# Kernel tuning notes

Measured on AMD Instinct MI355X. Metric: run time of the kernel, lower is better.

The kernel has to match this reference:

```python
import jax, jax.numpy as jnp
import numpy as np

DIM, N_HEADS, N_KV, HEAD_DIM = 3072, 24, 8, 128
N_REP = N_HEADS // N_KV  # 3
ROPE_THETA = 500000.0
B, S = 2, 2048


def _rope_tables(seqlen, head_dim, theta):
    inv = 1.0 / (theta ** (np.arange(0, head_dim, 2, dtype=np.float32) / head_dim))
    t = np.arange(seqlen, dtype=np.float32)
    ang = np.outer(t, inv)  # [S, head_dim//2]
    return jnp.asarray(np.cos(ang)), jnp.asarray(np.sin(ang))


def setup_inputs() -> dict:
    key = jax.random.key(0)
    ks = jax.random.split(key, 5)
    sd = 1.0 / np.sqrt(DIM)
    x = jax.random.normal(ks[0], (B, S, DIM), jnp.float32)
    wq = jax.random.normal(ks[1], (DIM, N_HEADS * HEAD_DIM), jnp.float32) * sd
    wk = jax.random.normal(ks[2], (DIM, N_KV * HEAD_DIM), jnp.float32) * sd
    wv = jax.random.normal(ks[3], (DIM, N_KV * HEAD_DIM), jnp.float32) * sd
    wo = jax.random.normal(ks[4], (N_HEADS * HEAD_DIM, DIM), jnp.float32) * sd
    fc, fs = _rope_tables(S, HEAD_DIM, ROPE_THETA)
    return {"x": x, "wq": wq, "wk": wk, "wv": wv, "wo": wo,
            "freqs_cos": fc, "freqs_sin": fs}


def _apply_rope(t, cos, sin):
    # t: [B,S,H,hd]; cos/sin: [S, hd//2]. Complex mult on (even, odd) pairs.
    tr = t[..., 0::2]
    ti = t[..., 1::2]
    cos = cos[None, :, None, :]
    sin = sin[None, :, None, :]
    out_r = tr * cos - ti * sin
    out_i = tr * sin + ti * cos
    return jnp.stack([out_r, out_i], axis=-1).reshape(t.shape)


def reference(x, wq, wk, wv, wo, freqs_cos, freqs_sin):
    b, s, _ = x.shape
    xq = (x @ wq).reshape(b, s, N_HEADS, HEAD_DIM)
    xk = (x @ wk).reshape(b, s, N_KV, HEAD_DIM)
    xv = (x @ wv).reshape(b, s, N_KV, HEAD_DIM)
    xq = _apply_rope(xq, freqs_cos, freqs_sin)
    xk = _apply_rope(xk, freqs_cos, freqs_sin)

    # GQA without materializing repeated k/v: q head h maps to kv group h // N_REP
    q = xq.reshape(b, s, N_KV, N_REP, HEAD_DIM)
    scale = 1.0 / np.sqrt(HEAD_DIM)
    scores = jnp.einsum('bsgrd,btgd->bgrst', q, xk) * scale  # [B,KV,rep,S,S]
    causal = jnp.tril(jnp.ones((s, s), dtype=bool))
    scores = jnp.where(causal[None, None, None], scores, jnp.finfo(scores.dtype).min)
    probs = jax.nn.softmax(scores, axis=-1)
    out = jnp.einsum('bgrst,btgd->bsgrd', probs, xv).reshape(b, s, N_HEADS * HEAD_DIM)
    return out @ wo
```

## Files before the change

### kernel.cpp

```cpp
#include <hip/hip_runtime.h>
#include <hip/hip_bf16.h>

typedef __hip_bfloat16 bf16;
typedef __bf16 bf16x8 __attribute__((ext_vector_type(8)));
typedef float f32x4 __attribute__((ext_vector_type(4)));
typedef short short8 __attribute__((ext_vector_type(8)));

#define NH 24
#define NKV 8
#define HD 128
#define SEQ 2048
#define NREP 3
#define QKVD 5120
#define KOFF 3072
#define VOFF 4096

__device__ inline void gload16(const void* g, void* l) {
  __builtin_amdgcn_global_load_lds(
      (const __attribute__((address_space(1))) void*)g,
      (__attribute__((address_space(3))) void*)l, 16, 0, 0);
}

__global__ void cast_f32_bf16(const float* __restrict__ in, bf16* __restrict__ out, int n4) {
  int i = blockIdx.x * 256 + threadIdx.x;
  if (i >= n4) return;
  float4 v = reinterpret_cast<const float4*>(in)[i];
  ushort4 u;
  u.x = __builtin_bit_cast(unsigned short, __float2bfloat16(v.x));
  u.y = __builtin_bit_cast(unsigned short, __float2bfloat16(v.y));
  u.z = __builtin_bit_cast(unsigned short, __float2bfloat16(v.z));
  u.w = __builtin_bit_cast(unsigned short, __float2bfloat16(v.w));
  reinterpret_cast<ushort4*>(out)[i] = u;
}

__global__ void transpose_cast(const float* __restrict__ W, bf16* __restrict__ WT, int K, int N) {
  __shared__ bf16 tile[32][33];
  int n0 = blockIdx.x * 32, k0 = blockIdx.y * 32;
  int tx = threadIdx.x, ty = threadIdx.y;
#pragma unroll
  for (int i = 0; i < 4; ++i) {
    int kl = ty + i * 8;
    tile[kl][tx] = __float2bfloat16(W[(size_t)(k0 + kl) * N + n0 + tx]);
  }
  __syncthreads();
#pragma unroll
  for (int i = 0; i < 4; ++i) {
    int nl = ty + i * 8;
    WT[(size_t)(n0 + nl) * K + k0 + tx] = tile[tx][nl];
  }
}

__global__ void transpose_v(const bf16* __restrict__ Vsrc, bf16* __restrict__ Vt) {
  __shared__ bf16 tile[32][33];
  int bg = blockIdx.z;
  int b = bg >> 3, g = bg & 7;
  int s0 = blockIdx.x * 32, d0 = blockIdx.y * 32;
  int tx = threadIdx.x, ty = threadIdx.y;
#pragma unroll
  for (int i = 0; i < 4; ++i) {
    int sl = ty + i * 8;
    tile[sl][tx] = Vsrc[(size_t)(b * SEQ + s0 + sl) * QKVD + g * HD + d0 + tx];
  }
  __syncthreads();
#pragma unroll
  for (int i = 0; i < 4; ++i) {
    int dl = ty + i * 8;
    Vt[((size_t)(b * NKV + g) * HD + d0 + dl) * SEQ + s0 + tx] = tile[tx][dl];
  }
}

__global__ void rope_kernel(bf16* __restrict__ T, const float* __restrict__ cosT,
                            const float* __restrict__ sinT, int H, int stride, int total) {
  int i = blockIdx.x * 256 + threadIdx.x;
  if (i >= total) return;
  int d2 = i & 63;
  int rh = i >> 6;
  int r = rh / H;
  int h = rh - r * H;
  int s = r & (SEQ - 1);
  float c = cosT[s * 64 + d2];
  float sn = sinT[s * 64 + d2];
  bf16* p = T + (size_t)r * stride + h * HD + d2 * 2;
  float a = __bfloat162float(p[0]);
  float b = __bfloat162float(p[1]);
  p[0] = __float2bfloat16(a * c - b * sn);
  p[1] = __float2bfloat16(a * sn + b * c);
}

#define QSLOT 14336
__global__ __launch_bounds__(512, 1) void gemm_qkv(const bf16* __restrict__ A,
                                                   const bf16* __restrict__ BT,
                                                   bf16* __restrict__ C,
                                                   int M, int N, int K, int gx) {
  extern __shared__ __align__(16) bf16 ls[];
  int nwg = gridDim.x;
  int flat = blockIdx.x;
  int swz = (flat & 7) * (nwg >> 3) + (flat >> 3);
  int bx = swz % gx, by = swz / gx;
  int m0 = by * 128, n0 = bx * 320;
  int tid = threadIdx.x, w = tid >> 6, lane = tid & 63;
  int wm = w >> 2, wn = w & 3;
  int lr = lane & 15, lk = lane >> 4;

  int aoff, adst;
  {
    int t = tid;
    int row = t >> 2, c = t & 3;
    aoff = row * K + ((c ^ ((row >> 1) & 3)) * 8);
    adst = t * 8;
  }
  const int nb = (tid < 256) ? 3 : 2;
  const int bbase = (tid < 256) ? tid : 768 + (tid - 256);
  int boff[3], bdst[3];
#pragma unroll
  for (int i = 0; i < 3; ++i) {
    int t = bbase + i * 256;
    if (t >= 1280) t = 0;
    int row = t >> 2, c = t & 3;
    boff[i] = row * K + ((c ^ ((row >> 1) & 3)) * 8);
    bdst[i] = 4096 + t * 8;
  }
  const bf16* Ab = A + (size_t)m0 * K;
  const bf16* Bb = BT + (size_t)n0 * K;

  auto STAGE_A = [&](int kt, int h, int slot) {
    const bf16* s = Ab + kt * 64 + h * 32;
    gload16(s + aoff, ls + slot * QSLOT + adst);
  };
  auto STAGE_B = [&](int kt, int h, int slot) {
    const bf16* s = Bb + kt * 64 + h * 32;
    bf16* d = ls + slot * QSLOT;
#pragma unroll
    for (int i = 0; i < 3; ++i)
      if (i < nb) gload16(s + boff[i], d + bdst[i]);
  };
  auto WAITN = [&] {
    if (tid < 256) asm volatile("s_waitcnt vmcnt(4)" ::: "memory");
    else           asm volatile("s_waitcnt vmcnt(3)" ::: "memory");
  };

  f32x4 acc[4][5] = {};
  bf16x8 aF[2], bF[5];

  auto LDA = [&](int slot, int mh) {
    const bf16* base = ls + slot * QSLOT;
#pragma unroll
    for (int mt = 0; mt < 2; ++mt) {
      int row = wm * 64 + (mh * 2 + mt) * 16 + lr;
      aF[mt] = *reinterpret_cast<const bf16x8*>(&base[row * 32 + ((lk ^ ((row >> 1) & 3)) * 8)]);
    }
  };
  auto LDB = [&](int slot) {
    const bf16* base = ls + slot * QSLOT + 4096;
#pragma unroll
    for (int nt = 0; nt < 5; ++nt) {
      int row = wn * 80 + nt * 16 + lr;
      bF[nt] = *reinterpret_cast<const bf16x8*>(&base[row * 32 + ((lk ^ ((row >> 1) & 3)) * 8)]);
    }
  };

#define PHASE(CSLOT, MH, STAGE_EXPR, DO_WAIT)                                       \
  {                                                                                 \
    __builtin_amdgcn_sched_barrier(0);                                              \
    if (MH == 0) LDB(CSLOT);                                                        \
    LDA(CSLOT, MH);                                                                 \
    STAGE_EXPR;                                                                     \
    __builtin_amdgcn_s_barrier();                                                   \
    asm volatile("s_waitcnt lgkmcnt(0)" ::: "memory");                              \
    __builtin_amdgcn_sched_barrier(0);                                              \
    __builtin_amdgcn_s_setprio(1);                                                  \
    _Pragma("unroll") for (int mt = 0; mt < 2; ++mt)                                \
        _Pragma("unroll") for (int nt = 0; nt < 5; ++nt)                            \
            acc[MH * 2 + mt][nt] =                                                  \
        __builtin_amdgcn_mfma_f32_16x16x32_bf16(aF[mt], bF[nt], acc[MH * 2 + mt][nt], 0, 0, 0); \
    __builtin_amdgcn_s_setprio(0);                                                  \
    if (DO_WAIT) WAITN();                                                           \
    __builtin_amdgcn_sched_barrier(0);                                              \
    __builtin_amdgcn_s_barrier();                                                   \
  }

  const int KT = K >> 6;
  const int IT = KT >> 1;

  STAGE_A(0, 0, 0); STAGE_B(0, 0, 0);
  STAGE_A(0, 1, 1); STAGE_B(0, 1, 1);
  STAGE_A(1, 0, 2); STAGE_B(1, 0, 2);
  WAITN();
  __builtin_amdgcn_s_barrier();

  for (int j = 0; j < IT; ++j) {
    int k1 = 2 * j + 1;
    int k2 = 2 * j + 2 < KT ? 2 * j + 2 : KT - 1;
    int k3 = 2 * j + 3 < KT ? 2 * j + 3 : KT - 1;
    PHASE(0, 0, STAGE_A(k1, 1, 3), false)
    PHASE(0, 1, STAGE_B(k1, 1, 3), false)
    PHASE(1, 0, STAGE_A(k2, 0, 0), false)
    PHASE(1, 1, STAGE_B(k2, 0, 0), true)
    PHASE(2, 0, STAGE_A(k2, 1, 1), false)
    PHASE(2, 1, STAGE_B(k2, 1, 1), false)
    PHASE(3, 0, STAGE_A(k3, 0, 2), false)
    PHASE(3, 1, STAGE_B(k3, 0, 2), true)
  }
  asm volatile("s_waitcnt vmcnt(0)" ::: "memory");
#undef PHASE

#pragma unroll
  for (int fr = 0; fr < 4; ++fr)
#pragma unroll
    for (int nt = 0; nt < 5; ++nt)
#pragma unroll
      for (int r = 0; r < 4; ++r) {
        int m = m0 + wm * 64 + fr * 16 + lk * 4 + r;
        int n = n0 + wn * 80 + nt * 16 + lr;
        C[(size_t)m * N + n] = __float2bfloat16(acc[fr][nt][r]);
      }
}

template <int NF, bool OUT_BF16>
__global__ __launch_bounds__(512, 1) void gemm_bt4(const bf16* __restrict__ A,
                                                   const bf16* __restrict__ BT,
                                                   void* __restrict__ Cv,
                                                   int M, int N, int K, int gx) {
  constexpr int BN = 64 * NF;
  constexpr int ASZ = 256 * 32;
  constexpr int BSZ = BN * 32;
  constexpr int SLOT = ASZ + BSZ;
  constexpr int HI = (NF + 1) / 2;
  extern __shared__ __align__(16) bf16 ls[];
  int nwg = gridDim.x;
  int flat = blockIdx.x;
  int swz = (flat & 7) * (nwg >> 3) + (flat >> 3);
  int bx = swz % gx, by = swz / gx;
  int m0 = by * 256, n0 = bx * BN;
  int tid = threadIdx.x, w = tid >> 6, lane = tid & 63;
  int wm = w >> 2, wn = w & 3;
  int lr = lane & 15, lk = lane >> 4;

  int aoff[2], adst[2];
#pragma unroll
  for (int i = 0; i < 2; ++i) {
    int t = i * 512 + tid;
    int row = t >> 2, c = t & 3;
    aoff[i] = row * K + ((c ^ ((row >> 1) & 3)) * 8);
    adst[i] = t * 8;
  }
  const int nb = (tid < 256) ? HI : NF / 2;
  const int bbase = (tid < 256) ? tid : HI * 256 + (tid - 256);
  int boff[HI], bdst[HI];
#pragma unroll
  for (int i = 0; i < HI; ++i) {
    int t = bbase + i * 256;
    if (t >= 256 * NF) t = 0;
    int row = t >> 2, c = t & 3;
    boff[i] = row * K + ((c ^ ((row >> 1) & 3)) * 8);
    bdst[i] = ASZ + t * 8;
  }
  const bf16* Ab = A + (size_t)m0 * K;
  const bf16* Bb = BT + (size_t)n0 * K;

  auto STAGE_A = [&](int kt, int h, int slot) {
    const bf16* s = Ab + kt * 64 + h * 32;
    bf16* d = ls + slot * SLOT;
#pragma unroll
    for (int i = 0; i < 2; ++i) gload16(s + aoff[i], d + adst[i]);
  };
  auto STAGE_B = [&](int kt, int h, int slot) {
    const bf16* s = Bb + kt * 64 + h * 32;
    bf16* d = ls + slot * SLOT;
#pragma unroll
    for (int i = 0; i < HI; ++i)
      if (i < nb) gload16(s + boff[i], d + bdst[i]);
  };
  auto WAITN = [&] {
    if (tid < 256) asm volatile("s_waitcnt vmcnt(4)" ::: "memory");
    else           asm volatile("s_waitcnt vmcnt(3)" ::: "memory");
  };

  f32x4 acc[8][NF] = {};
  bf16x8 aF[4], bF[NF];

  auto LDA = [&](int slot, int mh) {
    const bf16* base = ls + slot * SLOT;
#pragma unroll
    for (int mt = 0; mt < 4; ++mt) {
      int row = wm * 128 + (mh * 4 + mt) * 16 + lr;
      aF[mt] = *reinterpret_cast<const bf16x8*>(&base[row * 32 + ((lk ^ ((row >> 1) & 3)) * 8)]);
    }
  };
  auto LDB = [&](int slot) {
    const bf16* base = ls + slot * SLOT + ASZ;
#pragma unroll
    for (int nt = 0; nt < NF; ++nt) {
      int row = wn * (16 * NF) + nt * 16 + lr;
      bF[nt] = *reinterpret_cast<const bf16x8*>(&base[row * 32 + ((lk ^ ((row >> 1) & 3)) * 8)]);
    }
  };

#define PHASE(CSLOT, MH, STAGE_EXPR, DO_WAIT)                                       \
  {                                                                                 \
    __builtin_amdgcn_sched_barrier(0);                                              \
    if (MH == 0) LDB(CSLOT);                                                        \
    LDA(CSLOT, MH);                                                                 \
    STAGE_EXPR;                                                                     \
    __builtin_amdgcn_s_barrier();                                                   \
    asm volatile("s_waitcnt lgkmcnt(0)" ::: "memory");                              \
    __builtin_amdgcn_sched_barrier(0);                                              \
    __builtin_amdgcn_s_setprio(1);                                                  \
    _Pragma("unroll") for (int mt = 0; mt < 4; ++mt)                                \
        _Pragma("unroll") for (int nt = 0; nt < NF; ++nt)                           \
            acc[MH * 4 + mt][nt] =                                                  \
        __builtin_amdgcn_mfma_f32_16x16x32_bf16(aF[mt], bF[nt], acc[MH * 4 + mt][nt], 0, 0, 0); \
    __builtin_amdgcn_s_setprio(0);                                                  \
    if (DO_WAIT) WAITN();                                                           \
    __builtin_amdgcn_sched_barrier(0);                                              \
    __builtin_amdgcn_s_barrier();                                                   \
  }

  const int KT = K >> 6;
  const int IT = KT >> 1;

  STAGE_A(0, 0, 0); STAGE_B(0, 0, 0);
  STAGE_A(0, 1, 1); STAGE_B(0, 1, 1);
  STAGE_A(1, 0, 2); STAGE_B(1, 0, 2);
  WAITN();
  __builtin_amdgcn_s_barrier();

  for (int j = 0; j < IT; ++j) {
    int k1 = 2 * j + 1;
    int k2 = 2 * j + 2 < KT ? 2 * j + 2 : KT - 1;
    int k3 = 2 * j + 3 < KT ? 2 * j + 3 : KT - 1;
    PHASE(0, 0, STAGE_A(k1, 1, 3), false)
    PHASE(0, 1, STAGE_B(k1, 1, 3), false)
    PHASE(1, 0, STAGE_A(k2, 0, 0), false)
    PHASE(1, 1, STAGE_B(k2, 0, 0), true)
    PHASE(2, 0, STAGE_A(k2, 1, 1), false)
    PHASE(2, 1, STAGE_B(k2, 1, 1), false)
    PHASE(3, 0, STAGE_A(k3, 0, 2), false)
    PHASE(3, 1, STAGE_B(k3, 0, 2), true)
  }
  asm volatile("s_waitcnt vmcnt(0)" ::: "memory");
#undef PHASE

#pragma unroll
  for (int fr = 0; fr < 8; ++fr)
#pragma unroll
    for (int nt = 0; nt < NF; ++nt)
#pragma unroll
      for (int r = 0; r < 4; ++r) {
        int m = m0 + wm * 128 + fr * 16 + lk * 4 + r;
        int n = n0 + wn * (16 * NF) + nt * 16 + lr;
        float v = acc[fr][nt][r];
        if (OUT_BF16)
          reinterpret_cast<bf16*>(Cv)[(size_t)m * N + n] = __float2bfloat16(v);
        else
          reinterpret_cast<float*>(Cv)[(size_t)m * N + n] = v;
      }
}

#define SCALE_LOG2 0.12751745f

__global__ __launch_bounds__(256, 3) void attn_kernel(const bf16* __restrict__ QKV,
                                                      const bf16* __restrict__ Vt,
                                                      bf16* __restrict__ O) {
  __shared__ bf16 Klds[64 * 128];
  __shared__ bf16 Vlds[128 * 64];
  __shared__ bf16 Plds[4][16 * 64];
  int bh = blockIdx.y;
  int b = bh / NH, h = bh % NH, g = h / NREP;
  int tid = threadIdx.x, w = tid >> 6, lane = tid & 63;
  int lr = lane & 15, lk = lane >> 4;
  const int NT = SEQ / 64;

  const bf16* kvK = QKV + ((size_t)b * SEQ) * QKVD + KOFF + g * HD;
  const bf16* kvVt = Vt + ((size_t)(b * NKV + g) * HD) * SEQ;
  int koff[4];
  bf16* kdst[4];
#pragma unroll
  for (int i = 0; i < 4; ++i) {
    int t = i * 256 + tid;
    int row = t >> 4, c = t & 15;
    int sc = c ^ (row & 7);
    koff[i] = row * QKVD + sc * 8;
    kdst[i] = Klds + t * 8;
  }
  int voff[4];
  bf16* vdst[4];
#pragma unroll
  for (int i = 0; i < 4; ++i) {
    int t = i * 256 + tid;
    int d = t >> 3, c = t & 7;
    int sc = c ^ (d & 7);
    voff[i] = d * SEQ + sc * 8;
    vdst[i] = Vlds + t * 8;
  }

  bf16* pb = Plds[w];

#pragma unroll 1
  for (int pass = 0; pass < 2; ++pass) {
    int qt = pass ? (NT - 1 - (int)blockIdx.x) : (int)blockIdx.x;
    int q0 = qt * 64 + w * 16;

    bf16x8 aQ[4];
    {
      const bf16* qrow = QKV + ((size_t)(b * SEQ) + q0 + lr) * QKVD + h * HD;
#pragma unroll
      for (int kk = 0; kk < 4; ++kk)
        aQ[kk] = *reinterpret_cast<const bf16x8*>(qrow + kk * 32 + lk * 8);
    }

    f32x4 Oacc[8] = {};
    float m_s[4], l_s[4];
#pragma unroll
    for (int r = 0; r < 4; ++r) { m_s[r] = -1e30f; l_s[r] = 0.f; }

    int jlast = qt * 64;
    for (int j0 = 0; j0 <= jlast; j0 += 64) {
      __syncthreads();
      {
        const bf16* ks = kvK + (size_t)j0 * QKVD;
        const bf16* vs = kvVt + j0;
#pragma unroll
        for (int i = 0; i < 4; ++i) gload16(ks + koff[i], kdst[i]);
#pragma unroll
        for (int i = 0; i < 4; ++i) gload16(vs + voff[i], vdst[i]);
      }
      __syncthreads();
      if (j0 > q0 + 15) continue;

      f32x4 sc4[4] = {};
#pragma unroll
      for (int kk = 0; kk < 4; ++kk) {
#pragma unroll
        for (int nt = 0; nt < 4; ++nt) {
          int jrow = nt * 16 + lr;
          int pos = (4 * kk + lk) ^ (lr & 7);
          bf16x8 bK = *reinterpret_cast<const bf16x8*>(&Klds[jrow * 128 + pos * 8]);
          sc4[nt] = __builtin_amdgcn_mfma_f32_16x16x32_bf16(aQ[kk], bK, sc4[nt], 0, 0, 0);
        }
      }

      float sv[4][4], mx[4];
#pragma unroll
      for (int r = 0; r < 4; ++r) mx[r] = -3e38f;
#pragma unroll
      for (int nt = 0; nt < 4; ++nt) {
        int col = j0 + nt * 16 + lr;
#pragma unroll
        for (int r = 0; r < 4; ++r) {
          int row = q0 + lk * 4 + r;
          sv[nt][r] = (col > row) ? -3e38f : sc4[nt][r] * SCALE_LOG2;
          mx[r] = fmaxf(mx[r], sv[nt][r]);
        }
      }
#pragma unroll
      for (int d = 1; d < 16; d <<= 1)
#pragma unroll
        for (int r = 0; r < 4; ++r) mx[r] = fmaxf(mx[r], __shfl_xor(mx[r], d, 64));

      bool grow = false;
#pragma unroll
      for (int r = 0; r < 4; ++r) grow = grow || (mx[r] > m_s[r]);
      if (__any(grow)) {
        float alpha[4];
#pragma unroll
        for (int r = 0; r < 4; ++r) {
          float mn = fmaxf(m_s[r], mx[r]);
          alpha[r] = exp2f(m_s[r] - mn);
          m_s[r] = mn;
          l_s[r] *= alpha[r];
        }
#pragma unroll
        for (int nc = 0; nc < 8; ++nc)
#pragma unroll
          for (int r = 0; r < 4; ++r) Oacc[nc][r] *= alpha[r];
      }
      float p[4][4], rs[4];
#pragma unroll
      for (int r = 0; r < 4; ++r) {
        rs[r] = 0.f;
#pragma unroll
        for (int nt = 0; nt < 4; ++nt) {
          p[nt][r] = exp2f(sv[nt][r] - m_s[r]);
          rs[r] += p[nt][r];
        }
      }
#pragma unroll
      for (int d = 1; d < 16; d <<= 1)
#pragma unroll
        for (int r = 0; r < 4; ++r) rs[r] += __shfl_xor(rs[r], d, 64);
#pragma unroll
      for (int r = 0; r < 4; ++r) l_s[r] += rs[r];

#pragma unroll
      for (int nt = 0; nt < 4; ++nt)
#pragma unroll
        for (int r = 0; r < 4; ++r) {
          int row = lk * 4 + r;
          int c = nt * 16 + lr;
          pb[row * 64 + (((c >> 3) ^ (row & 7)) * 8) + (c & 7)] = __float2bfloat16(p[nt][r]);
        }
      asm volatile("s_waitcnt lgkmcnt(0)" ::: "memory");
      __builtin_amdgcn_sched_barrier(0);

#pragma unroll
      for (int kb = 0; kb < 2; ++kb) {
        int px = ((kb * 4 + lk) ^ (lr & 7)) * 8;
        bf16x8 aP = *reinterpret_cast<const bf16x8*>(&pb[lr * 64 + px]);
#pragma unroll
        for (int nc = 0; nc < 8; ++nc) {
          bf16x8 bV = *reinterpret_cast<const bf16x8*>(&Vlds[(nc * 16 + lr) * 64 + px]);
          Oacc[nc] = __builtin_amdgcn_mfma_f32_16x16x32_bf16(aP, bV, Oacc[nc], 0, 0, 0);
        }
      }
    }

#pragma unroll
    for (int r = 0; r < 4; ++r) {
      float inv = 1.0f / l_s[r];
      size_t rowoff = ((size_t)(b * SEQ) + q0 + lk * 4 + r) * (NH * HD) + h * HD;
#pragma unroll
      for (int nc = 0; nc < 8; ++nc)
        O[rowoff + nc * 16 + lr] = __float2bfloat16(Oacc[nc][r] * inv);
    }
  }
}

extern "C" void kernel_launch(void* const* d_in, const int* in_sizes, int n_in,
                              void* d_out, int out_size, void* d_ws, size_t ws_size,
                              hipStream_t stream) {
  const float* x = (const float*)d_in[0];
  const float* wq = (const float*)d_in[1];
  const float* wk = (const float*)d_in[2];
  const float* wv = (const float*)d_in[3];
  const float* wo = (const float*)d_in[4];
  const float* fc = (const float*)d_in[5];
  const float* fs = (const float*)d_in[6];
  float* out = (float*)d_out;
  (void)in_sizes; (void)n_in; (void)out_size; (void)ws_size;

  const int R = 2 * SEQ;
  const int DIMc = 3072;
  const int NQ = NH * HD;

  char* ws = (char*)d_ws;
  bf16* xb = (bf16*)ws;     ws += (size_t)R * DIMc * 2;
  bf16* wqkvT = (bf16*)ws;  ws += (size_t)QKVD * DIMc * 2;
  bf16* woT = (bf16*)ws;    ws += (size_t)DIMc * NQ * 2;
  bf16* QKVb = (bf16*)ws;   ws += (size_t)R * QKVD * 2;
  bf16* Ob = (bf16*)ws;     ws += (size_t)R * NQ * 2;
  bf16* VtG = xb;

  const int LDSQ = 4 * QSLOT * 2;
  const int LDSB3 = 4 * (256 * 32 + 192 * 32) * 2;
  hipFuncSetAttribute((const void*)gemm_qkv,
                      hipFuncAttributeMaxDynamicSharedMemorySize, LDSQ);
  hipFuncSetAttribute((const void*)gemm_bt4<3, false>,
                      hipFuncAttributeMaxDynamicSharedMemorySize, LDSB3);

  {
    int n4 = R * DIMc / 4;
    cast_f32_bf16<<<n4 / 256, 256, 0, stream>>>(x, xb, n4);
  }
  transpose_cast<<<dim3(NQ / 32, DIMc / 32), dim3(32, 8), 0, stream>>>(wq, wqkvT, DIMc, NQ);
  transpose_cast<<<dim3(1024 / 32, DIMc / 32), dim3(32, 8), 0, stream>>>(
      wk, wqkvT + (size_t)KOFF * DIMc, DIMc, 1024);
  transpose_cast<<<dim3(1024 / 32, DIMc / 32), dim3(32, 8), 0, stream>>>(
      wv, wqkvT + (size_t)VOFF * DIMc, DIMc, 1024);
  transpose_cast<<<dim3(DIMc / 32, NQ / 32), dim3(32, 8), 0, stream>>>(wo, woT, NQ, DIMc);
  gemm_qkv<<<(QKVD / 320) * (R / 128), 512, LDSQ, stream>>>(
      xb, wqkvT, QKVb, R, QKVD, DIMc, QKVD / 320);
  transpose_v<<<dim3(SEQ / 32, HD / 32, 2 * NKV), dim3(32, 8), 0, stream>>>(QKVb + VOFF, VtG);
  {
    int totQ = R * NH * 64;
    rope_kernel<<<totQ / 256, 256, 0, stream>>>(QKVb, fc, fs, NH, QKVD, totQ);
    int totK = R * NKV * 64;
    rope_kernel<<<totK / 256, 256, 0, stream>>>(QKVb + KOFF, fc, fs, NKV, QKVD, totK);
  }
  attn_kernel<<<dim3(SEQ / 128, 2 * NH), 256, 0, stream>>>(QKVb, VtG, Ob);
  gemm_bt4<3, false><<<(DIMc / 192) * (R / 256), 512, LDSB3, stream>>>(
      Ob, woT, out, R, DIMc, NQ, DIMc / 192);
}
```

Before: 422.3 us.

## Fuse RoPE into QKV GEMM epilogue and transpose attention score layout

Applies rotary embedding inside the QKV GEMM epilogue, pairing even and odd columns with a lane shuffle. This removes the two separate rope kernels and their extra read-modify-write pass over Q and K. The attention kernel also swaps the MFMA operand order so each lane holds one query row. That turns the row max and row sum reductions into two shuffles on scalars, and s_setprio is raised around the MFMA blocks. The cost is that the GEMM epilogue now does cos/sin global loads and a shuffle per element, and correctness depends on adjacent columns sitting in adjacent lanes.

```diff
diff --git a/kernel.cpp b/kernel.cpp
--- a/kernel.cpp
+++ b/kernel.cpp
@@ -69,28 +69,12 @@
   }
 }
 
-__global__ void rope_kernel(bf16* __restrict__ T, const float* __restrict__ cosT,
-                            const float* __restrict__ sinT, int H, int stride, int total) {
-  int i = blockIdx.x * 256 + threadIdx.x;
-  if (i >= total) return;
-  int d2 = i & 63;
-  int rh = i >> 6;
-  int r = rh / H;
-  int h = rh - r * H;
-  int s = r & (SEQ - 1);
-  float c = cosT[s * 64 + d2];
-  float sn = sinT[s * 64 + d2];
-  bf16* p = T + (size_t)r * stride + h * HD + d2 * 2;
-  float a = __bfloat162float(p[0]);
-  float b = __bfloat162float(p[1]);
-  p[0] = __float2bfloat16(a * c - b * sn);
-  p[1] = __float2bfloat16(a * sn + b * c);
-}
-
 #define QSLOT 14336
 __global__ __launch_bounds__(512, 1) void gemm_qkv(const bf16* __restrict__ A,
                                                    const bf16* __restrict__ BT,
                                                    bf16* __restrict__ C,
+                                                   const float* __restrict__ fcos,
+                                                   const float* __restrict__ fsin,
                                                    int M, int N, int K, int gx) {
   extern __shared__ __align__(16) bf16 ls[];
   int nwg = gridDim.x;
@@ -212,7 +196,16 @@
       for (int r = 0; r < 4; ++r) {
         int m = m0 + wm * 64 + fr * 16 + lk * 4 + r;
         int n = n0 + wn * 80 + nt * 16 + lr;
-        C[(size_t)m * N + n] = __float2bfloat16(acc[fr][nt][r]);
+        float v = acc[fr][nt][r];
+        float part = __shfl_xor(v, 1, 64);
+        if (n < VOFF) {
+          int s = m & (SEQ - 1);
+          int d2 = (n & (HD - 1)) >> 1;
+          float c = fcos[s * 64 + d2];
+          float sn = fsin[s * 64 + d2];
+          v = (n & 1) ? (part * sn + v * c) : (v * c - part * sn);
+        }
+        C[(size_t)m * N + n] = __float2bfloat16(v);
       }
 }
 
@@ -400,19 +393,18 @@
   for (int pass = 0; pass < 2; ++pass) {
     int qt = pass ? (NT - 1 - (int)blockIdx.x) : (int)blockIdx.x;
     int q0 = qt * 64 + w * 16;
+    int qrow = q0 + lr;
 
     bf16x8 aQ[4];
     {
-      const bf16* qrow = QKV + ((size_t)(b * SEQ) + q0 + lr) * QKVD + h * HD;
+      const bf16* qrp = QKV + ((size_t)(b * SEQ) + q0 + lr) * QKVD + h * HD;
 #pragma unroll
       for (int kk = 0; kk < 4; ++kk)
-        aQ[kk] = *reinterpret_cast<const bf16x8*>(qrow + kk * 32 + lk * 8);
+        aQ[kk] = *reinterpret_cast<const bf16x8*>(qrp + kk * 32 + lk * 8);
     }
 
     f32x4 Oacc[8] = {};
-    float m_s[4], l_s[4];
-#pragma unroll
-    for (int r = 0; r < 4; ++r) { m_s[r] = -1e30f; l_s[r] = 0.f; }
+    float m_s = -1e30f, l_s = 0.f;
 
     int jlast = qt * 64;
     for (int j0 = 0; j0 <= jlast; j0 += 64) {
@@ -429,6 +421,7 @@
       if (j0 > q0 + 15) continue;
 
       f32x4 sc4[4] = {};
+      __builtin_amdgcn_s_setprio(1);
 #pragma unroll
       for (int kk = 0; kk < 4; ++kk) {
 #pragma unroll
@@ -436,73 +429,59 @@
           int jrow = nt * 16 + lr;
           int pos = (4 * kk + lk) ^ (lr & 7);
           bf16x8 bK = *reinterpret_cast<const bf16x8*>(&Klds[jrow * 128 + pos * 8]);
-          sc4[nt] = __builtin_amdgcn_mfma_f32_16x16x32_bf16(aQ[kk], bK, sc4[nt], 0, 0, 0);
+          sc4[nt] = __builtin_amdgcn_mfma_f32_16x16x32_bf16(bK, aQ[kk], sc4[nt], 0, 0, 0);
         }
       }
-
-      float sv[4][4], mx[4];
-#pragma unroll
-      for (int r = 0; r < 4; ++r) mx[r] = -3e38f;
-#pragma unroll
-      for (int nt = 0; nt < 4; ++nt) {
-        int col = j0 + nt * 16 + lr;
+      __builtin_amdgcn_s_setprio(0);
+
+      float sv[4][4], mxl = -3e38f;
+#pragma unroll
+      for (int nt = 0; nt < 4; ++nt)
 #pragma unroll
         for (int r = 0; r < 4; ++r) {
-          int row = q0 + lk * 4 + r;
-          sv[nt][r] = (col > row) ? -3e38f : sc4[nt][r] * SCALE_LOG2;
-          mx[r] = fmaxf(mx[r], sv[nt][r]);
+          int col = j0 + nt * 16 + lk * 4 + r;
+          sv[nt][r] = (col > qrow) ? -3e38f : sc4[nt][r] * SCALE_LOG2;
+          mxl = fmaxf(mxl, sv[nt][r]);
         }
+      mxl = fmaxf(mxl, __shfl_xor(mxl, 16, 64));
+      mxl = fmaxf(mxl, __shfl_xor(mxl, 32, 64));
+
+      if (__any(mxl > m_s)) {
+        float mn = fmaxf(m_s, mxl);
+        float alpha = exp2f(m_s - mn);
+        m_s = mn;
+        l_s *= alpha;
+        float ar[4];
+#pragma unroll
+        for (int r = 0; r < 4; ++r) ar[r] = __shfl(alpha, lk * 4 + r, 16);
+#pragma unroll
+        for (int nc = 0; nc < 8; ++nc)
+#pragma unroll
+          for (int r = 0; r < 4; ++r) Oacc[nc][r] *= ar[r];
       }
-#pragma unroll
-      for (int d = 1; d < 16; d <<= 1)
-#pragma unroll
-        for (int r = 0; r < 4; ++r) mx[r] = fmaxf(mx[r], __shfl_xor(mx[r], d, 64));
-
-      bool grow = false;
-#pragma unroll
-      for (int r = 0; r < 4; ++r) grow = grow || (mx[r] > m_s[r]);
-      if (__any(grow)) {
-        float alpha[4];
+      float p[4][4], rsl = 0.f;
+#pragma unroll
+      for (int nt = 0; nt < 4; ++nt)
 #pragma unroll
         for (int r = 0; r < 4; ++r) {
-          float mn = fmaxf(m_s[r], mx[r]);
-          alpha[r] = exp2f(m_s[r] - mn);
-          m_s[r] = mn;
-          l_s[r] *= alpha[r];
+          p[nt][r] = exp2f(sv[nt][r] - m_s);
+          rsl += p[nt][r];
         }
-#pragma unroll
-        for (int nc = 0; nc < 8; ++nc)
-#pragma unroll
-          for (int r = 0; r < 4; ++r) Oacc[nc][r] *= alpha[r];
-      }
-      float p[4][4], rs[4];
-#pragma unroll
-      for (int r = 0; r < 4; ++r) {
-        rs[r] = 0.f;
-#pragma unroll
-        for (int nt = 0; nt < 4; ++nt) {
-          p[nt][r] = exp2f(sv[nt][r] - m_s[r]);
-          rs[r] += p[nt][r];
-        }
-      }
-#pragma unroll
-      for (int d = 1; d < 16; d <<= 1)
-#pragma unroll
-        for (int r = 0; r < 4; ++r) rs[r] += __shfl_xor(rs[r], d, 64);
-#pragma unroll
-      for (int r = 0; r < 4; ++r) l_s[r] += rs[r];
+      rsl += __shfl_xor(rsl, 16, 64);
+      rsl += __shfl_xor(rsl, 32, 64);
+      l_s += rsl;
 
 #pragma unroll
       for (int nt = 0; nt < 4; ++nt)
 #pragma unroll
         for (int r = 0; r < 4; ++r) {
-          int row = lk * 4 + r;
-          int c = nt * 16 + lr;
-          pb[row * 64 + (((c >> 3) ^ (row & 7)) * 8) + (c & 7)] = __float2bfloat16(p[nt][r]);
+          int c = nt * 16 + lk * 4 + r;
+          pb[lr * 64 + (((c >> 3) ^ (lr & 7)) * 8) + (c & 7)] = __float2bfloat16(p[nt][r]);
         }
       asm volatile("s_waitcnt lgkmcnt(0)" ::: "memory");
       __builtin_amdgcn_sched_barrier(0);
 
+      __builtin_amdgcn_s_setprio(1);
 #pragma unroll
       for (int kb = 0; kb < 2; ++kb) {
         int px = ((kb * 4 + lk) ^ (lr & 7)) * 8;
@@ -513,15 +492,19 @@
           Oacc[nc] = __builtin_amdgcn_mfma_f32_16x16x32_bf16(aP, bV, Oacc[nc], 0, 0, 0);
         }
       }
-    }
-
+      __builtin_amdgcn_s_setprio(0);
+    }
+
+    float linv = 1.0f / l_s;
+    float inv_r[4];
+#pragma unroll
+    for (int r = 0; r < 4; ++r) inv_r[r] = __shfl(linv, lk * 4 + r, 16);
 #pragma unroll
     for (int r = 0; r < 4; ++r) {
-      float inv = 1.0f / l_s[r];
       size_t rowoff = ((size_t)(b * SEQ) + q0 + lk * 4 + r) * (NH * HD) + h * HD;
 #pragma unroll
       for (int nc = 0; nc < 8; ++nc)
-        O[rowoff + nc * 16 + lr] = __float2bfloat16(Oacc[nc][r] * inv);
+        O[rowoff + nc * 16 + lr] = __float2bfloat16(Oacc[nc][r] * inv_r[r]);
     }
   }
 }
@@ -569,14 +552,8 @@
       wv, wqkvT + (size_t)VOFF * DIMc, DIMc, 1024);
   transpose_cast<<<dim3(DIMc / 32, NQ / 32), dim3(32, 8), 0, stream>>>(wo, woT, NQ, DIMc);
   gemm_qkv<<<(QKVD / 320) * (R / 128), 512, LDSQ, stream>>>(
-      xb, wqkvT, QKVb, R, QKVD, DIMc, QKVD / 320);
+      xb, wqkvT, QKVb, fc, fs, R, QKVD, DIMc, QKVD / 320);
   transpose_v<<<dim3(SEQ / 32, HD / 32, 2 * NKV), dim3(32, 8), 0, stream>>>(QKVb + VOFF, VtG);
-  {
-    int totQ = R * NH * 64;
-    rope_kernel<<<totQ / 256, 256, 0, stream>>>(QKVb, fc, fs, NH, QKVD, totQ);
-    int totK = R * NKV * 64;
-    rope_kernel<<<totK / 256, 256, 0, stream>>>(QKVb + KOFF, fc, fs, NKV, QKVD, totK);
-  }
   attn_kernel<<<dim3(SEQ / 128, 2 * NH), 256, 0, stream>>>(QKVb, VtG, Ob);
   gemm_bt4<3, false><<<(DIMc / 192) * (R / 256), 512, LDSB3, stream>>>(
       Ob, woT, out, R, DIMc, NQ, DIMc / 192);
```

Measured after the change: 404.3 us. 4.3% less time.
